# Kernel optimization log

Measured on AMD Instinct MI355X. Metric: run time of the kernel, lower is better.

Reference implementation:

```python
import jax, jax.numpy as jnp
import numpy as np

B, T, C = 2, 2048, 1024
H = 16
DH = C // H  # 64
DFF = 4 * C  # 4096
EPS = 1e-5


def layernorm(x, gamma, beta):
    # torch.var defaults to unbiased (ddof=1) -- replicate exactly
    m = jnp.mean(x, axis=-1, keepdims=True)
    v = jnp.var(x, axis=-1, ddof=1, keepdims=True)
    return (x - m) / jnp.sqrt(v + EPS) * gamma + beta


def setup_inputs() -> dict:
    key = jax.random.key(0)
    ks = jax.random.split(key, 12)
    s = 0.02
    return {
        "x": jax.random.normal(ks[0], (B, T, C), jnp.float32),
        "Wq": jax.random.normal(ks[1], (H, C, DH), jnp.float32) * s,
        "bq": jnp.zeros((H, DH), jnp.float32),
        "Wk": jax.random.normal(ks[2], (H, C, DH), jnp.float32) * s,
        "bk": jnp.zeros((H, DH), jnp.float32),
        "Wv": jax.random.normal(ks[3], (H, C, DH), jnp.float32) * s,
        "bv": jnp.zeros((H, DH), jnp.float32),
        "Wo": jax.random.normal(ks[4], (C, C), jnp.float32) * s,
        "bo": jnp.zeros((C,), jnp.float32),
        "gamma1": jnp.ones((C,), jnp.float32),
        "beta1": jnp.zeros((C,), jnp.float32),
        "gamma2": jnp.ones((C,), jnp.float32),
        "beta2": jnp.zeros((C,), jnp.float32),
        "W1": jax.random.normal(ks[5], (C, DFF), jnp.float32) * s,
        "b1": jnp.zeros((DFF,), jnp.float32),
        "W2": jax.random.normal(ks[6], (DFF, C), jnp.float32) * s,
        "b2": jnp.zeros((C,), jnp.float32),
    }


def reference(x, Wq, bq, Wk, bk, Wv, bv, Wo, bo,
              gamma1, beta1, gamma2, beta2, W1, b1, W2, b2):
    Tn = x.shape[1]
    # Block: x = ln1(x); x = x + attn(x); x = ln2(x); out = x + ffw(x)
    x = layernorm(x, gamma1, beta1)

    # per-head Q/K/V linears, stacked over heads: [B,T,C] x [H,C,Dh] -> [B,H,T,Dh]
    q = jnp.einsum('btc,hcd->bhtd', x, Wq) + bq[None, :, None, :]
    k = jnp.einsum('btc,hcd->bhtd', x, Wk) + bk[None, :, None, :]
    v = jnp.einsum('btc,hcd->bhtd', x, Wv) + bv[None, :, None, :]

    scale = DH ** -0.5
    scores = jnp.einsum('bhtd,bhsd->bhts', q, k) * scale  # [B,H,T,T]
    causal = jnp.tril(jnp.ones((Tn, Tn), dtype=bool))
    scores = jnp.where(causal, scores, -jnp.inf)
    alpha = jax.nn.softmax(scores, axis=-1)
    h = jnp.einsum('bhts,bhsd->bhtd', alpha, v)  # [B,H,T,Dh]
    h = jnp.transpose(h, (0, 2, 1, 3)).reshape(x.shape)  # concat heads -> [B,T,C]
    attn_out = h @ Wo + bo

    x = x + attn_out
    x = layernorm(x, gamma2, beta2)
    ffw = jax.nn.gelu(x @ W1 + b1, approximate=False) @ W2 + b2
    return x + ffw
```

## Files before the change

kernel.cpp:

```cpp
#include <hip/hip_runtime.h>

typedef unsigned short u16;
typedef unsigned int u32;
typedef __attribute__((ext_vector_type(8))) short bf16x8;
typedef __attribute__((ext_vector_type(4))) float f32x4;

#define AS1 __attribute__((address_space(1)))
#define AS3 __attribute__((address_space(3)))

__device__ __forceinline__ u16 f2bf(float f) {
  u32 u = __float_as_uint(f);
  u = (u + 0x7fffu + ((u >> 16) & 1u)) >> 16;
  return (u16)u;
}
__device__ __forceinline__ float bf2f(u16 v) { return __uint_as_float((u32)v << 16); }

__device__ __forceinline__ void gl16(const void* g, void* l) {
  __builtin_amdgcn_global_load_lds((AS1 void*)g, (AS3 void*)l, 16, 0, 0);
}

__device__ __forceinline__ float exp2a(float x) {
  float r;
  asm("v_exp_f32 %0, %1" : "=v"(r) : "v"(x));
  return r;
}
__device__ __forceinline__ u32 pk2(float lo, float hi) {
  u32 r;
  asm("v_cvt_pk_bf16_f32 %0, %1, %2" : "=v"(r) : "v"(lo), "v"(hi));
  return r;
}

#define LGKM0()                                         \
  do {                                                  \
    asm volatile("s_waitcnt lgkmcnt(0)" ::: "memory");  \
    __builtin_amdgcn_sched_barrier(0);                  \
  } while (0)
#define VMC0()                                          \
  do {                                                  \
    asm volatile("s_waitcnt vmcnt(0)" ::: "memory");    \
    __builtin_amdgcn_sched_barrier(0);                  \
  } while (0)

__global__ __launch_bounds__(256) void ln_kernel(const float* __restrict__ in,
                                                 const float* __restrict__ gamma,
                                                 const float* __restrict__ beta,
                                                 u16* __restrict__ obf,
                                                 float* __restrict__ of32) {
  const int row = blockIdx.x;
  const int tid = threadIdx.x;
  const float* xr = in + (long)row * 1024;
  float4 v = *(const float4*)(xr + tid * 4);
  float s = v.x + v.y + v.z + v.w;
  float sq = v.x * v.x + v.y * v.y + v.z * v.z + v.w * v.w;
#pragma unroll
  for (int off = 1; off < 64; off <<= 1) {
    s += __shfl_xor(s, off);
    sq += __shfl_xor(sq, off);
  }
  __shared__ float rs[4], rq[4];
  const int w = tid >> 6, lane = tid & 63;
  if (lane == 0) { rs[w] = s; rq[w] = sq; }
  __syncthreads();
  s = rs[0] + rs[1] + rs[2] + rs[3];
  sq = rq[0] + rq[1] + rq[2] + rq[3];
  const float mean = s * (1.0f / 1024.0f);
  const float var = (sq - 1024.0f * mean * mean) * (1.0f / 1023.0f);
  const float rstd = rsqrtf(var + 1e-5f);
  float4 g4 = *(const float4*)(gamma + tid * 4);
  float4 b4 = *(const float4*)(beta + tid * 4);
  float o0 = (v.x - mean) * rstd * g4.x + b4.x;
  float o1 = (v.y - mean) * rstd * g4.y + b4.y;
  float o2 = (v.z - mean) * rstd * g4.z + b4.z;
  float o3 = (v.w - mean) * rstd * g4.w + b4.w;
  *(float4*)(of32 + (long)row * 1024 + tid * 4) = make_float4(o0, o1, o2, o3);
  ushort4 ub;
  ub.x = f2bf(o0); ub.y = f2bf(o1); ub.z = f2bf(o2); ub.w = f2bf(o3);
  *(ushort4*)(obf + (long)row * 1024 + tid * 4) = ub;
}

__global__ __launch_bounds__(256) void ln2_fused_kernel(
    const u16* __restrict__ p0, const u16* __restrict__ p1,
    const float* __restrict__ bo, const float* __restrict__ xn,
    const float* __restrict__ gamma, const float* __restrict__ beta,
    u16* __restrict__ obf, float* __restrict__ of32) {
  const int row = blockIdx.x;
  const int tid = threadIdx.x;
  const long i4 = (long)row * 1024 + tid * 4;
  ushort4 a0 = *(const ushort4*)(p0 + i4);
  ushort4 a1 = *(const ushort4*)(p1 + i4);
  float4 xv = *(const float4*)(xn + i4);
  float4 bv = *(const float4*)(bo + tid * 4);
  float y0 = bf2f(a0.x) + bf2f(a1.x) + bv.x + xv.x;
  float y1 = bf2f(a0.y) + bf2f(a1.y) + bv.y + xv.y;
  float y2 = bf2f(a0.z) + bf2f(a1.z) + bv.z + xv.z;
  float y3 = bf2f(a0.w) + bf2f(a1.w) + bv.w + xv.w;
  float s = y0 + y1 + y2 + y3;
  float sq = y0 * y0 + y1 * y1 + y2 * y2 + y3 * y3;
#pragma unroll
  for (int off = 1; off < 64; off <<= 1) {
    s += __shfl_xor(s, off);
    sq += __shfl_xor(sq, off);
  }
  __shared__ float rs[4], rq[4];
  const int w = tid >> 6, lane = tid & 63;
  if (lane == 0) { rs[w] = s; rq[w] = sq; }
  __syncthreads();
  s = rs[0] + rs[1] + rs[2] + rs[3];
  sq = rq[0] + rq[1] + rq[2] + rq[3];
  const float mean = s * (1.0f / 1024.0f);
  const float var = (sq - 1024.0f * mean * mean) * (1.0f / 1023.0f);
  const float rstd = rsqrtf(var + 1e-5f);
  float4 g4 = *(const float4*)(gamma + tid * 4);
  float4 b4 = *(const float4*)(beta + tid * 4);
  float o0 = (y0 - mean) * rstd * g4.x + b4.x;
  float o1 = (y1 - mean) * rstd * g4.y + b4.y;
  float o2 = (y2 - mean) * rstd * g4.z + b4.z;
  float o3 = (y3 - mean) * rstd * g4.w + b4.w;
  *(float4*)(of32 + i4) = make_float4(o0, o1, o2, o3);
  ushort4 ub;
  ub.x = f2bf(o0); ub.y = f2bf(o1); ub.z = f2bf(o2); ub.w = f2bf(o3);
  *(ushort4*)(obf + i4) = ub;
}

__global__ __launch_bounds__(256) void wprep_kernel(
    const float* __restrict__ Wq, const float* __restrict__ Wk,
    const float* __restrict__ Wv, const float* __restrict__ Wo,
    const float* __restrict__ W1, const float* __restrict__ W2,
    u16* __restrict__ WqkvT, u16* __restrict__ WoT,
    u16* __restrict__ W1T, u16* __restrict__ W2T) {
  __shared__ float tile[32][33];
  int id = blockIdx.x;
  const float* ip;
  u16* op;
  int in_rs, R, c0, r0;
  if (id < 3072) {
    const int x = id & 1, y = (id >> 1) & 31, z = id >> 6;
    const float* in = z < 16 ? Wq : (z < 32 ? Wk : Wv);
    ip = in + (long)(z & 15) * 65536;
    op = WqkvT + (long)z * 65536;
    in_rs = 64; R = 1024; c0 = x * 32; r0 = y * 32;
  } else if (id < 4096) {
    id -= 3072;
    ip = Wo; op = WoT; in_rs = 1024; R = 1024;
    c0 = (id & 31) * 32; r0 = (id >> 5) * 32;
  } else if (id < 8192) {
    id -= 4096;
    ip = W1; op = W1T; in_rs = 4096; R = 1024;
    c0 = (id & 127) * 32; r0 = (id >> 7) * 32;
  } else {
    id -= 8192;
    ip = W2; op = W2T; in_rs = 1024; R = 4096;
    c0 = (id & 31) * 32; r0 = (id >> 5) * 32;
  }
  const int tx = threadIdx.x, ty = threadIdx.y;
#pragma unroll
  for (int i = 0; i < 4; ++i)
    tile[ty + i * 8][tx] = ip[(long)(r0 + ty + i * 8) * in_rs + c0 + tx];
  __syncthreads();
#pragma unroll
  for (int i = 0; i < 4; ++i)
    op[(long)(c0 + ty + i * 8) * R + r0 + tx] = f2bf(tile[tx][ty + i * 8]);
}

__global__ __launch_bounds__(256) void ffn2_reduce_kernel(const u16* __restrict__ p,
                                                          const float* __restrict__ b2,
                                                          const float* __restrict__ yn,
                                                          float* __restrict__ out) {
  const long i4 = ((long)blockIdx.x * 256 + threadIdx.x) * 4;
  ushort4 p0 = *(const ushort4*)(p + i4);
  ushort4 p1 = *(const ushort4*)(p + 4194304 + i4);
  float4 rr = *(const float4*)(yn + i4);
  const int nn = (int)(i4 & 1023);
  float4 bb = *(const float4*)(b2 + nn);
  float4 o;
  o.x = bf2f(p0.x) + bf2f(p1.x) + bb.x + rr.x;
  o.y = bf2f(p0.y) + bf2f(p1.y) + bb.y + rr.y;
  o.z = bf2f(p0.z) + bf2f(p1.z) + bb.z + rr.z;
  o.w = bf2f(p0.w) + bf2f(p1.w) + bb.w + rr.w;
  *(float4*)(out + i4) = o;
}

template <int EPI>
__global__ __launch_bounds__(256, 2) void gemm128_kernel(
    const u16* __restrict__ A, const u16* __restrict__ Bt,
    int K, int nk, int N,
    const float* bias0, const float* bias1, const float* bias2,
    void* out0, void* out1) {
  __shared__ __align__(16) u16 Asm[128 * 64];
  __shared__ __align__(16) u16 Bsm[128 * 64];
  const int tid = threadIdx.x;
  const int lane = tid & 63, w = tid >> 6;
  const int wm = w >> 1, wn = w & 1;
  const int q = lane & 15, g = lane >> 4;
  const long m0 = (long)blockIdx.x * 128;
  const long n0 = (long)blockIdx.y * 128;
  const int bz = blockIdx.z;
  const long koff = (long)bz * (long)nk * 64;

  f32x4 zero4 = {0.f, 0.f, 0.f, 0.f};
  f32x4 acc[4][4];
#pragma unroll
  for (int mi = 0; mi < 4; ++mi)
#pragma unroll
    for (int ni = 0; ni < 4; ++ni) acc[mi][ni] = zero4;

  for (int ks = 0; ks < nk; ++ks) {
    __syncthreads();
    const u16* ga = A + m0 * K + koff + ks * 64;
    const u16* gb = Bt + n0 * K + koff + ks * 64;
    const int base = w * 256;
#pragma unroll
    for (int i = 0; i < 4; ++i) {
      const int idx = base + i * 64 + lane;
      const int row = idx >> 3;
      const int lg = (idx & 7) ^ (row & 7);
      gl16(ga + (long)row * K + lg * 8, Asm + (long)(base + i * 64) * 8);
    }
#pragma unroll
    for (int i = 0; i < 4; ++i) {
      const int idx = base + i * 64 + lane;
      const int row = idx >> 3;
      const int lg = (idx & 7) ^ (row & 7);
      gl16(gb + (long)row * K + lg * 8, Bsm + (long)(base + i * 64) * 8);
    }
    __syncthreads();
#pragma unroll
    for (int half = 0; half < 2; ++half) {
      bf16x8 af[4], bfv[4];
#pragma unroll
      for (int mi = 0; mi < 4; ++mi) {
        const int row = wm * 64 + mi * 16 + q;
        const int ph = (half * 4 + g) ^ (row & 7);
        af[mi] = *(const bf16x8*)(Asm + row * 64 + ph * 8);
      }
#pragma unroll
      for (int ni = 0; ni < 4; ++ni) {
        const int row = wn * 64 + ni * 16 + q;
        const int ph = (half * 4 + g) ^ (row & 7);
        bfv[ni] = *(const bf16x8*)(Bsm + row * 64 + ph * 8);
      }
#pragma unroll
      for (int mi = 0; mi < 4; ++mi)
#pragma unroll
        for (int ni = 0; ni < 4; ++ni)
          acc[mi][ni] = __builtin_amdgcn_mfma_f32_16x16x32_bf16(af[mi], bfv[ni],
                                                                acc[mi][ni], 0, 0, 0);
    }
  }
#pragma unroll
  for (int mi = 0; mi < 4; ++mi) {
#pragma unroll
    for (int ni = 0; ni < 4; ++ni) {
      const long mbase = m0 + wm * 64 + mi * 16 + 4 * g;
      const long n = n0 + wn * 64 + ni * 16 + q;
      f32x4 a = acc[mi][ni];
      if constexpr (EPI == 0) {
        const int sel = (int)(n >> 10);
        const int nn = (int)(n & 1023);
        const float* bp = sel == 0 ? bias0 : (sel == 1 ? bias1 : bias2);
        const float bb2 = bp[nn];
        if (sel < 2) {
          const float sc = (sel == 0) ? 0.18033688011112043f : 1.0f;
          u16* qkp = (u16*)out0;
#pragma unroll
          for (int r = 0; r < 4; ++r)
            qkp[(mbase + r) * 2048 + n] = f2bf((a[r] + bb2) * sc);
        } else {
          const int bI = (int)(mbase >> 11);
          const int t = (int)(mbase & 2047);
          const int hh = nn >> 6, dh = nn & 63;
          ushort4 pk;
          pk.x = f2bf(a[0] + bb2); pk.y = f2bf(a[1] + bb2);
          pk.z = f2bf(a[2] + bb2); pk.w = f2bf(a[3] + bb2);
          *(ushort4*)((u16*)out1 + ((long)((bI * 16 + hh) * 64 + dh)) * 2048 + t) = pk;
        }
      } else if constexpr (EPI == 2) {
        u16* gp = (u16*)out0;
        const float bb2 = bias0[(int)n];
#pragma unroll
        for (int r = 0; r < 4; ++r) {
          const float xg = a[r] + bb2;
          const float ge = 0.5f * xg * (1.0f + erff(xg * 0.70710678118f));
          gp[(mbase + r) * N + n] = f2bf(ge);
        }
      } else {
        u16* pp = (u16*)out0 + (long)bz * 4096 * 1024;
#pragma unroll
        for (int r = 0; r < 4; ++r) pp[(mbase + r) * 1024 + n] = f2bf(a[r]);
      }
    }
  }
}

__device__ __forceinline__ void attn_stage(const u16* kbase, const u16* vtb, int kb,
                                           u16* Kd, u16* Vd, int tid) {
#pragma unroll
  for (int it = 0; it < 2; ++it) {
    const int gi = it * 256 + tid;
    const int row = gi >> 3;
    const int lg = (gi & 7) ^ (row & 7);
    gl16(kbase + (long)(kb * 64 + row) * 2048 + lg * 8, Kd + gi * 8);
    gl16(vtb + (long)row * 2048 + kb * 64 + lg * 8, Vd + gi * 8);
  }
}

__device__ __forceinline__ void softmax_slab(const f32x4 st[4], bool diag, int qrow,
                                             int kb, int g, int q15,
                                             float& m2, float& l, u16* prow,
                                             float al[4]) {
  float sv[4][4];
  float rmax = -1e30f;
#pragma unroll
  for (int sub = 0; sub < 4; ++sub)
#pragma unroll
    for (int r = 0; r < 4; ++r) {
      float s_ = st[sub][r];
      if (diag) {
        const int key = kb * 64 + sub * 16 + 4 * g + r;
        s_ = (key > qrow) ? -1e30f : s_;
      }
      sv[sub][r] = s_;
      rmax = fmaxf(rmax, s_);
    }
  rmax = fmaxf(rmax, __shfl_xor(rmax, 16));
  rmax = fmaxf(rmax, __shfl_xor(rmax, 32));
  const float mnew = fmaxf(m2, rmax);
  const float alpha = exp2a(m2 - mnew);
  float psum = 0.f;
#pragma unroll
  for (int sub = 0; sub < 4; ++sub) {
    const float p0 = exp2a(sv[sub][0] - mnew);
    const float p1 = exp2a(sv[sub][1] - mnew);
    const float p2 = exp2a(sv[sub][2] - mnew);
    const float p3 = exp2a(sv[sub][3] - mnew);
    uint2 u;
    u.x = pk2(p0, p1);
    u.y = pk2(p2, p3);
    *(uint2*)(prow + sub * 16 + 4 * g) = u;
    psum += (p0 + p1) + (p2 + p3);
  }
  psum += __shfl_xor(psum, 16);
  psum += __shfl_xor(psum, 32);
  l = l * alpha + psum;
  m2 = mnew;
#pragma unroll
  for (int r = 0; r < 4; ++r) al[r] = __shfl(alpha, 4 * g + r);
}

__global__ __launch_bounds__(256, 2) void attn_kernel(const u16* __restrict__ qk,
                                                      const u16* __restrict__ vT,
                                                      u16* __restrict__ o) {
  __shared__ __align__(16) u16 Ksm[2][64 * 64];
  __shared__ __align__(16) u16 Vsm[2][64 * 64];
  __shared__ __align__(16) u16 Psm[8][16][72];
  const int lid = blockIdx.x;
  const int xcd = lid & 7, s6 = lid >> 3;
  const int b2 = (s6 >> 4) & 3, xr = s6 & 15;
  const int qs = (b2 & 2) ? (15 - xr) : xr;
  const int bh = xcd + 8 * b2;
  const int b = bh >> 4, h = bh & 15;
  const int tid = threadIdx.x, lane = tid & 63, w = tid >> 6;
  const int q15 = lane & 15, g = lane >> 4;
  const u16* qbase = qk + (long)b * 2048 * 2048 + h * 64;
  const u16* kbase = qbase + 1024;
  const u16* vtb = vT + (long)bh * 64 * 2048;
  f32x4 zero4 = {0.f, 0.f, 0.f, 0.f};

  const int r0 = qs * 128 + w * 16 + q15;
  bf16x8 qa[2][2];
  qa[0][0] = *(const bf16x8*)(qbase + (long)r0 * 2048 + g * 8);
  qa[0][1] = *(const bf16x8*)(qbase + (long)r0 * 2048 + 32 + g * 8);
  qa[1][0] = *(const bf16x8*)(qbase + (long)(r0 + 64) * 2048 + g * 8);
  qa[1][1] = *(const bf16x8*)(qbase + (long)(r0 + 64) * 2048 + 32 + g * 8);

  f32x4 oa0[4], oa1[4];
#pragma unroll
  for (int dv = 0; dv < 4; ++dv) { oa0[dv] = zero4; oa1[dv] = zero4; }
  float m20 = -1e30f, l0 = 0.f, m21 = -1e30f, l1 = 0.f;
  const int kbmax = 2 * qs + 1;

  attn_stage(kbase, vtb, 0, Ksm[0], Vsm[0], tid);
  VMC0();
  __syncthreads();

  for (int kb = 0; kb <= kbmax; ++kb) {
    const int buf = kb & 1;
    if (kb < kbmax) attn_stage(kbase, vtb, kb + 1, Ksm[buf ^ 1], Vsm[buf ^ 1], tid);
    const u16* Kb = Ksm[buf];
    const u16* Vb = Vsm[buf];
    const bool s0on = (kb <= 2 * qs);
    f32x4 st0[4], st1[4];
#pragma unroll
    for (int sub = 0; sub < 4; ++sub) {
      const int row = sub * 16 + q15;
      const bf16x8 ka0 = *(const bf16x8*)(Kb + row * 64 + ((g ^ (row & 7)) * 8));
      const bf16x8 ka1 = *(const bf16x8*)(Kb + row * 64 + (((4 + g) ^ (row & 7)) * 8));
      f32x4 z = zero4;
      z = __builtin_amdgcn_mfma_f32_16x16x32_bf16(ka0, qa[1][0], z, 0, 0, 0);
      z = __builtin_amdgcn_mfma_f32_16x16x32_bf16(ka1, qa[1][1], z, 0, 0, 0);
      st1[sub] = z;
      if (s0on) {
        f32x4 z0 = zero4;
        z0 = __builtin_amdgcn_mfma_f32_16x16x32_bf16(ka0, qa[0][0], z0, 0, 0, 0);
        z0 = __builtin_amdgcn_mfma_f32_16x16x32_bf16(ka1, qa[0][1], z0, 0, 0, 0);
        st0[sub] = z0;
      }
    }
    float al0[4], al1[4];
    if (s0on)
      softmax_slab(st0, kb == 2 * qs, r0, kb, g, q15, m20, l0, &Psm[w * 2][q15][0], al0);
    softmax_slab(st1, kb == 2 * qs + 1, r0 + 64, kb, g, q15, m21, l1,
                 &Psm[w * 2 + 1][q15][0], al1);
    if (s0on)
#pragma unroll
      for (int dv = 0; dv < 4; ++dv) {
        oa0[dv][0] *= al0[0]; oa0[dv][1] *= al0[1];
        oa0[dv][2] *= al0[2]; oa0[dv][3] *= al0[3];
      }
#pragma unroll
    for (int dv = 0; dv < 4; ++dv) {
      oa1[dv][0] *= al1[0]; oa1[dv][1] *= al1[1];
      oa1[dv][2] *= al1[2]; oa1[dv][3] *= al1[3];
    }
    LGKM0();
#pragma unroll
    for (int half = 0; half < 2; ++half) {
      const bf16x8 pa0 = *(const bf16x8*)(&Psm[w * 2][q15][half * 32 + 8 * g]);
      const bf16x8 pa1 = *(const bf16x8*)(&Psm[w * 2 + 1][q15][half * 32 + 8 * g]);
#pragma unroll
      for (int dv = 0; dv < 4; ++dv) {
        const int row = dv * 16 + q15;
        const bf16x8 vb = *(const bf16x8*)(Vb + row * 64 + (((half * 4 + g) ^ (row & 7)) * 8));
        if (s0on) oa0[dv] = __builtin_amdgcn_mfma_f32_16x16x32_bf16(pa0, vb, oa0[dv], 0, 0, 0);
        oa1[dv] = __builtin_amdgcn_mfma_f32_16x16x32_bf16(pa1, vb, oa1[dv], 0, 0, 0);
      }
    }
    VMC0();
    __syncthreads();
  }
  const float li0 = 1.0f / l0, li1 = 1.0f / l1;
  float v0[4], v1[4];
#pragma unroll
  for (int r = 0; r < 4; ++r) {
    v0[r] = __shfl(li0, 4 * g + r);
    v1[r] = __shfl(li1, 4 * g + r);
  }
  const int tok0 = b * 2048 + qs * 128 + w * 16;
#pragma unroll
  for (int dv = 0; dv < 4; ++dv)
#pragma unroll
    for (int r = 0; r < 4; ++r) {
      o[(long)(tok0 + 4 * g + r) * 1024 + h * 64 + dv * 16 + q15] =
          f2bf(oa0[dv][r] * v0[r]);
      o[(long)(tok0 + 64 + 4 * g + r) * 1024 + h * 64 + dv * 16 + q15] =
          f2bf(oa1[dv][r] * v1[r]);
    }
}

extern "C" void kernel_launch(void* const* d_in, const int* in_sizes, int n_in,
                              void* d_out, int out_size, void* d_ws, size_t ws_size,
                              hipStream_t stream) {
  (void)in_sizes; (void)n_in; (void)out_size; (void)ws_size;
  const float* x  = (const float*)d_in[0];
  const float* Wq = (const float*)d_in[1];
  const float* bq = (const float*)d_in[2];
  const float* Wk = (const float*)d_in[3];
  const float* bk = (const float*)d_in[4];
  const float* Wv = (const float*)d_in[5];
  const float* bv = (const float*)d_in[6];
  const float* Wo = (const float*)d_in[7];
  const float* bo = (const float*)d_in[8];
  const float* g1 = (const float*)d_in[9];
  const float* be1 = (const float*)d_in[10];
  const float* g2 = (const float*)d_in[11];
  const float* be2 = (const float*)d_in[12];
  const float* W1 = (const float*)d_in[13];
  const float* b1 = (const float*)d_in[14];
  const float* W2 = (const float*)d_in[15];
  const float* b2 = (const float*)d_in[16];

  char* ws = (char*)d_ws;
  u16*   xn_bf = (u16*)  (ws + 0);
  float* xn_f  = (float*)(ws + 8388608);
  u16*   WqkvT = (u16*)  (ws + 25165824);
  u16*   WoT   = (u16*)  (ws + 31457280);
  u16*   W1T   = (u16*)  (ws + 33554432);
  u16*   W2T   = (u16*)  (ws + 41943040);
  u16*   qkb   = (u16*)  (ws + 50331648);
  u16*   vTb   = (u16*)  (ws + 67108864);
  u16*   ah    = (u16*)  (ws + 75497472);
  u16*   pwo0  = (u16*)  (ws + 50331648);
  u16*   gbuf  = (u16*)  (ws + 50331648);
  u16*   part  = (u16*)  (ws + 0);
  u16*   yn_bf = (u16*)  (ws + 83886080);
  float* yn_f  = (float*)(ws + 92274688);

  dim3 tb(32, 8), b256(256);
  wprep_kernel<<<dim3(12288), tb, 0, stream>>>(Wq, Wk, Wv, Wo, W1, W2,
                                               WqkvT, WoT, W1T, W2T);
  ln_kernel<<<dim3(4096), b256, 0, stream>>>(x, g1, be1, xn_bf, xn_f);
  gemm128_kernel<0><<<dim3(32, 24, 1), b256, 0, stream>>>(xn_bf, WqkvT, 1024, 16, 3072,
                                                          bq, bk, bv, qkb, vTb);
  attn_kernel<<<dim3(512), b256, 0, stream>>>(qkb, vTb, ah);
  gemm128_kernel<5><<<dim3(32, 8, 2), b256, 0, stream>>>(ah, WoT, 1024, 8, 1024,
                                                         nullptr, nullptr, nullptr, pwo0, nullptr);
  ln2_fused_kernel<<<dim3(4096), b256, 0, stream>>>(pwo0, pwo0 + 4194304, bo, xn_f,
                                                    g2, be2, yn_bf, yn_f);
  gemm128_kernel<2><<<dim3(32, 32, 1), b256, 0, stream>>>(yn_bf, W1T, 1024, 16, 4096,
                                                          b1, nullptr, nullptr, gbuf, nullptr);
  gemm128_kernel<5><<<dim3(32, 8, 2), b256, 0, stream>>>(gbuf, W2T, 4096, 32, 1024,
                                                         nullptr, nullptr, nullptr, part, nullptr);
  ffn2_reduce_kernel<<<dim3(4096), b256, 0, stream>>>(part, b2, yn_f, (float*)d_out);
}
```

Measured before the change: 216.4 us.

## Fuse LN1 into weight-prep launch and drop fp32 residual copies

```diff
diff --git a/kernel.cpp b/kernel.cpp
--- a/kernel.cpp
+++ b/kernel.cpp
@@ -41,104 +41,57 @@
     __builtin_amdgcn_sched_barrier(0);                  \
   } while (0)
 
-__global__ __launch_bounds__(256) void ln_kernel(const float* __restrict__ in,
-                                                 const float* __restrict__ gamma,
-                                                 const float* __restrict__ beta,
-                                                 u16* __restrict__ obf,
-                                                 float* __restrict__ of32) {
-  const int row = blockIdx.x;
-  const int tid = threadIdx.x;
-  const float* xr = in + (long)row * 1024;
-  float4 v = *(const float4*)(xr + tid * 4);
-  float s = v.x + v.y + v.z + v.w;
-  float sq = v.x * v.x + v.y * v.y + v.z * v.z + v.w * v.w;
-#pragma unroll
-  for (int off = 1; off < 64; off <<= 1) {
-    s += __shfl_xor(s, off);
-    sq += __shfl_xor(sq, off);
-  }
-  __shared__ float rs[4], rq[4];
-  const int w = tid >> 6, lane = tid & 63;
-  if (lane == 0) { rs[w] = s; rq[w] = sq; }
-  __syncthreads();
-  s = rs[0] + rs[1] + rs[2] + rs[3];
-  sq = rq[0] + rq[1] + rq[2] + rq[3];
-  const float mean = s * (1.0f / 1024.0f);
-  const float var = (sq - 1024.0f * mean * mean) * (1.0f / 1023.0f);
-  const float rstd = rsqrtf(var + 1e-5f);
-  float4 g4 = *(const float4*)(gamma + tid * 4);
-  float4 b4 = *(const float4*)(beta + tid * 4);
-  float o0 = (v.x - mean) * rstd * g4.x + b4.x;
-  float o1 = (v.y - mean) * rstd * g4.y + b4.y;
-  float o2 = (v.z - mean) * rstd * g4.z + b4.z;
-  float o3 = (v.w - mean) * rstd * g4.w + b4.w;
-  *(float4*)(of32 + (long)row * 1024 + tid * 4) = make_float4(o0, o1, o2, o3);
-  ushort4 ub;
-  ub.x = f2bf(o0); ub.y = f2bf(o1); ub.z = f2bf(o2); ub.w = f2bf(o3);
-  *(ushort4*)(obf + (long)row * 1024 + tid * 4) = ub;
-}
-
-__global__ __launch_bounds__(256) void ln2_fused_kernel(
-    const u16* __restrict__ p0, const u16* __restrict__ p1,
-    const float* __restrict__ bo, const float* __restrict__ xn,
-    const float* __restrict__ gamma, const float* __restrict__ beta,
-    u16* __restrict__ obf, float* __restrict__ of32) {
-  const int row = blockIdx.x;
-  const int tid = threadIdx.x;
-  const long i4 = (long)row * 1024 + tid * 4;
-  ushort4 a0 = *(const ushort4*)(p0 + i4);
-  ushort4 a1 = *(const ushort4*)(p1 + i4);
-  float4 xv = *(const float4*)(xn + i4);
-  float4 bv = *(const float4*)(bo + tid * 4);
-  float y0 = bf2f(a0.x) + bf2f(a1.x) + bv.x + xv.x;
-  float y1 = bf2f(a0.y) + bf2f(a1.y) + bv.y + xv.y;
-  float y2 = bf2f(a0.z) + bf2f(a1.z) + bv.z + xv.z;
-  float y3 = bf2f(a0.w) + bf2f(a1.w) + bv.w + xv.w;
-  float s = y0 + y1 + y2 + y3;
-  float sq = y0 * y0 + y1 * y1 + y2 * y2 + y3 * y3;
-#pragma unroll
-  for (int off = 1; off < 64; off <<= 1) {
-    s += __shfl_xor(s, off);
-    sq += __shfl_xor(sq, off);
-  }
-  __shared__ float rs[4], rq[4];
-  const int w = tid >> 6, lane = tid & 63;
-  if (lane == 0) { rs[w] = s; rq[w] = sq; }
-  __syncthreads();
-  s = rs[0] + rs[1] + rs[2] + rs[3];
-  sq = rq[0] + rq[1] + rq[2] + rq[3];
-  const float mean = s * (1.0f / 1024.0f);
-  const float var = (sq - 1024.0f * mean * mean) * (1.0f / 1023.0f);
-  const float rstd = rsqrtf(var + 1e-5f);
-  float4 g4 = *(const float4*)(gamma + tid * 4);
-  float4 b4 = *(const float4*)(beta + tid * 4);
-  float o0 = (y0 - mean) * rstd * g4.x + b4.x;
-  float o1 = (y1 - mean) * rstd * g4.y + b4.y;
-  float o2 = (y2 - mean) * rstd * g4.z + b4.z;
-  float o3 = (y3 - mean) * rstd * g4.w + b4.w;
-  *(float4*)(of32 + i4) = make_float4(o0, o1, o2, o3);
-  ushort4 ub;
-  ub.x = f2bf(o0); ub.y = f2bf(o1); ub.z = f2bf(o2); ub.w = f2bf(o3);
-  *(ushort4*)(obf + i4) = ub;
-}
-
 __global__ __launch_bounds__(256) void wprep_kernel(
     const float* __restrict__ Wq, const float* __restrict__ Wk,
     const float* __restrict__ Wv, const float* __restrict__ Wo,
     const float* __restrict__ W1, const float* __restrict__ W2,
     u16* __restrict__ WqkvT, u16* __restrict__ WoT,
-    u16* __restrict__ W1T, u16* __restrict__ W2T) {
+    u16* __restrict__ W1T, u16* __restrict__ W2T,
+    const float* __restrict__ x, const float* __restrict__ gamma,
+    const float* __restrict__ beta, u16* __restrict__ xn_bf) {
   __shared__ float tile[32][33];
+  __shared__ float rs[4], rq[4];
   int id = blockIdx.x;
+  const int tx = threadIdx.x, ty = threadIdx.y;
+  if (id >= 12288) {
+    const int row = id - 12288;
+    const int tid = ty * 32 + tx;
+    const float* xr = x + (long)row * 1024;
+    float4 v = *(const float4*)(xr + tid * 4);
+    float s = v.x + v.y + v.z + v.w;
+    float sq = v.x * v.x + v.y * v.y + v.z * v.z + v.w * v.w;
+#pragma unroll
+    for (int off = 1; off < 64; off <<= 1) {
+      s += __shfl_xor(s, off);
+      sq += __shfl_xor(sq, off);
+    }
+    const int w = tid >> 6, lane = tid & 63;
+    if (lane == 0) { rs[w] = s; rq[w] = sq; }
+    __syncthreads();
+    s = rs[0] + rs[1] + rs[2] + rs[3];
+    sq = rq[0] + rq[1] + rq[2] + rq[3];
+    const float mean = s * (1.0f / 1024.0f);
+    const float var = (sq - 1024.0f * mean * mean) * (1.0f / 1023.0f);
+    const float rstd = rsqrtf(var + 1e-5f);
+    float4 g4 = *(const float4*)(gamma + tid * 4);
+    float4 b4 = *(const float4*)(beta + tid * 4);
+    ushort4 ub;
+    ub.x = f2bf((v.x - mean) * rstd * g4.x + b4.x);
+    ub.y = f2bf((v.y - mean) * rstd * g4.y + b4.y);
+    ub.z = f2bf((v.z - mean) * rstd * g4.z + b4.z);
+    ub.w = f2bf((v.w - mean) * rstd * g4.w + b4.w);
+    *(ushort4*)(xn_bf + (long)row * 1024 + tid * 4) = ub;
+    return;
+  }
   const float* ip;
   u16* op;
   int in_rs, R, c0, r0;
   if (id < 3072) {
-    const int x = id & 1, y = (id >> 1) & 31, z = id >> 6;
+    const int xq = id & 1, y = (id >> 1) & 31, z = id >> 6;
     const float* in = z < 16 ? Wq : (z < 32 ? Wk : Wv);
     ip = in + (long)(z & 15) * 65536;
     op = WqkvT + (long)z * 65536;
-    in_rs = 64; R = 1024; c0 = x * 32; r0 = y * 32;
+    in_rs = 64; R = 1024; c0 = xq * 32; r0 = y * 32;
   } else if (id < 4096) {
     id -= 3072;
     ip = Wo; op = WoT; in_rs = 1024; R = 1024;
@@ -152,7 +105,6 @@
     ip = W2; op = W2T; in_rs = 1024; R = 4096;
     c0 = (id & 31) * 32; r0 = (id >> 5) * 32;
   }
-  const int tx = threadIdx.x, ty = threadIdx.y;
 #pragma unroll
   for (int i = 0; i < 4; ++i)
     tile[ty + i * 8][tx] = ip[(long)(r0 + ty + i * 8) * in_rs + c0 + tx];
@@ -162,21 +114,63 @@
     op[(long)(c0 + ty + i * 8) * R + r0 + tx] = f2bf(tile[tx][ty + i * 8]);
 }
 
+__global__ __launch_bounds__(256) void ln2_fused_kernel(
+    const u16* __restrict__ p0, const u16* __restrict__ p1,
+    const float* __restrict__ bo, const u16* __restrict__ xnbf,
+    const float* __restrict__ gamma, const float* __restrict__ beta,
+    u16* __restrict__ obf) {
+  const int row = blockIdx.x;
+  const int tid = threadIdx.x;
+  const long i4 = (long)row * 1024 + tid * 4;
+  ushort4 a0 = *(const ushort4*)(p0 + i4);
+  ushort4 a1 = *(const ushort4*)(p1 + i4);
+  ushort4 xv = *(const ushort4*)(xnbf + i4);
+  float4 bv = *(const float4*)(bo + tid * 4);
+  float y0 = bf2f(a0.x) + bf2f(a1.x) + bv.x + bf2f(xv.x);
+  float y1 = bf2f(a0.y) + bf2f(a1.y) + bv.y + bf2f(xv.y);
+  float y2 = bf2f(a0.z) + bf2f(a1.z) + bv.z + bf2f(xv.z);
+  float y3 = bf2f(a0.w) + bf2f(a1.w) + bv.w + bf2f(xv.w);
+  float s = y0 + y1 + y2 + y3;
+  float sq = y0 * y0 + y1 * y1 + y2 * y2 + y3 * y3;
+#pragma unroll
+  for (int off = 1; off < 64; off <<= 1) {
+    s += __shfl_xor(s, off);
+    sq += __shfl_xor(sq, off);
+  }
+  __shared__ float rs[4], rq[4];
+  const int w = tid >> 6, lane = tid & 63;
+  if (lane == 0) { rs[w] = s; rq[w] = sq; }
+  __syncthreads();
+  s = rs[0] + rs[1] + rs[2] + rs[3];
+  sq = rq[0] + rq[1] + rq[2] + rq[3];
+  const float mean = s * (1.0f / 1024.0f);
+  const float var = (sq - 1024.0f * mean * mean) * (1.0f / 1023.0f);
+  const float rstd = rsqrtf(var + 1e-5f);
+  float4 g4 = *(const float4*)(gamma + tid * 4);
+  float4 b4 = *(const float4*)(beta + tid * 4);
+  ushort4 ub;
+  ub.x = f2bf((y0 - mean) * rstd * g4.x + b4.x);
+  ub.y = f2bf((y1 - mean) * rstd * g4.y + b4.y);
+  ub.z = f2bf((y2 - mean) * rstd * g4.z + b4.z);
+  ub.w = f2bf((y3 - mean) * rstd * g4.w + b4.w);
+  *(ushort4*)(obf + i4) = ub;
+}
+
 __global__ __launch_bounds__(256) void ffn2_reduce_kernel(const u16* __restrict__ p,
                                                           const float* __restrict__ b2,
-                                                          const float* __restrict__ yn,
+                                                          const u16* __restrict__ ynbf,
                                                           float* __restrict__ out) {
   const long i4 = ((long)blockIdx.x * 256 + threadIdx.x) * 4;
   ushort4 p0 = *(const ushort4*)(p + i4);
   ushort4 p1 = *(const ushort4*)(p + 4194304 + i4);
-  float4 rr = *(const float4*)(yn + i4);
+  ushort4 rr = *(const ushort4*)(ynbf + i4);
   const int nn = (int)(i4 & 1023);
   float4 bb = *(const float4*)(b2 + nn);
   float4 o;
-  o.x = bf2f(p0.x) + bf2f(p1.x) + bb.x + rr.x;
-  o.y = bf2f(p0.y) + bf2f(p1.y) + bb.y + rr.y;
-  o.z = bf2f(p0.z) + bf2f(p1.z) + bb.z + rr.z;
-  o.w = bf2f(p0.w) + bf2f(p1.w) + bb.w + rr.w;
+  o.x = bf2f(p0.x) + bf2f(p1.x) + bb.x + bf2f(rr.x);
+  o.y = bf2f(p0.y) + bf2f(p1.y) + bb.y + bf2f(rr.y);
+  o.z = bf2f(p0.z) + bf2f(p1.z) + bb.z + bf2f(rr.z);
+  o.w = bf2f(p0.w) + bf2f(p1.w) + bb.w + bf2f(rr.w);
   *(float4*)(out + i4) = o;
 }
 
@@ -481,7 +475,6 @@
 
   char* ws = (char*)d_ws;
   u16*   xn_bf = (u16*)  (ws + 0);
-  float* xn_f  = (float*)(ws + 8388608);
   u16*   WqkvT = (u16*)  (ws + 25165824);
   u16*   WoT   = (u16*)  (ws + 31457280);
   u16*   W1T   = (u16*)  (ws + 33554432);
@@ -491,24 +484,23 @@
   u16*   ah    = (u16*)  (ws + 75497472);
   u16*   pwo0  = (u16*)  (ws + 50331648);
   u16*   gbuf  = (u16*)  (ws + 50331648);
-  u16*   part  = (u16*)  (ws + 0);
+  u16*   part  = (u16*)  (ws + 8388608);
   u16*   yn_bf = (u16*)  (ws + 83886080);
-  float* yn_f  = (float*)(ws + 92274688);
 
   dim3 tb(32, 8), b256(256);
-  wprep_kernel<<<dim3(12288), tb, 0, stream>>>(Wq, Wk, Wv, Wo, W1, W2,
-                                               WqkvT, WoT, W1T, W2T);
-  ln_kernel<<<dim3(4096), b256, 0, stream>>>(x, g1, be1, xn_bf, xn_f);
+  wprep_kernel<<<dim3(16384), tb, 0, stream>>>(Wq, Wk, Wv, Wo, W1, W2,
+                                               WqkvT, WoT, W1T, W2T,
+                                               x, g1, be1, xn_bf);
   gemm128_kernel<0><<<dim3(32, 24, 1), b256, 0, stream>>>(xn_bf, WqkvT, 1024, 16, 3072,
                                                           bq, bk, bv, qkb, vTb);
   attn_kernel<<<dim3(512), b256, 0, stream>>>(qkb, vTb, ah);
   gemm128_kernel<5><<<dim3(32, 8, 2), b256, 0, stream>>>(ah, WoT, 1024, 8, 1024,
                                                          nullptr, nullptr, nullptr, pwo0, nullptr);
-  ln2_fused_kernel<<<dim3(4096), b256, 0, stream>>>(pwo0, pwo0 + 4194304, bo, xn_f,
-                                                    g2, be2, yn_bf, yn_f);
+  ln2_fused_kernel<<<dim3(4096), b256, 0, stream>>>(pwo0, pwo0 + 4194304, bo, xn_bf,
+                                                    g2, be2, yn_bf);
   gemm128_kernel<2><<<dim3(32, 32, 1), b256, 0, stream>>>(yn_bf, W1T, 1024, 16, 4096,
                                                           b1, nullptr, nullptr, gbuf, nullptr);
   gemm128_kernel<5><<<dim3(32, 8, 2), b256, 0, stream>>>(gbuf, W2T, 4096, 32, 1024,
                                                          nullptr, nullptr, nullptr, part, nullptr);
-  ffn2_reduce_kernel<<<dim3(4096), b256, 0, stream>>>(part, b2, yn_f, (float*)d_out);
-}
+  ffn2_reduce_kernel<<<dim3(4096), b256, 0, stream>>>(part, b2, yn_bf, (float*)d_out);
+}
```

Result: faster. 208.8 us (median of 2 runs) (-3.5%).
